# Kernel tuning notes

Hardware: AMD Instinct MI355X
Metric: run time of the kernel (lower is better)

The kernel has to match this reference:

```python
import jax, jax.numpy as jnp
import numpy as np

# SMPL kinematic tree (24 joints); parent[0] = -1 (root)
PARENT = [-1, 0, 0, 0, 1, 2, 3, 4, 5, 6, 7, 8, 9, 9, 9, 12, 13, 14, 16, 17, 18, 19, 20, 21]
J = len(PARENT)  # 24


def _ancestor_matrix(parent):
    # A[j, k] = 1 if offset k contributes to joint j (k on path root->j, excluding root)
    n = len(parent)
    A = np.zeros((n, n), dtype=np.float32)
    for j in range(1, n):
        k = j
        while k > 0:
            A[j, k] = 1.0
            k = parent[k]
    return A

ANC = jnp.asarray(_ancestor_matrix(PARENT))  # [J, J]


def setup_inputs() -> dict:
    key = jax.random.key(0)
    k0, k1, k2 = jax.random.split(key, 3)
    B, D, H = 131072, 256, 512
    out_dim = (J - 1) * 4
    z = jax.random.normal(k0, (B, D), jnp.float32)
    W1 = jax.random.normal(k1, (D, H), jnp.float32) / np.float32(np.sqrt(D))
    b1 = jnp.zeros((H,), jnp.float32)
    W2 = jax.random.normal(k2, (H, out_dim), jnp.float32) / np.float32(np.sqrt(H))
    b2 = jnp.zeros((out_dim,), jnp.float32)
    return {"z": z, "W1": W1, "b1": b1, "W2": W2, "b2": b2}


def reference(z, W1, b1, W2, b2):
    B = z.shape[0]
    h = jax.nn.silu(z @ W1 + b1)                      # [B, 512]
    raw = (h @ W2 + b2).reshape(B, J - 1, 4)          # [B, J-1, 4]
    dir_raw = raw[..., :3]                            # [B, J-1, 3]
    len_raw = raw[..., 3]                             # [B, J-1]
    # F.normalize(dim=-1, eps=1e-6): x / max(||x||, eps)
    norm = jnp.linalg.norm(dir_raw, axis=-1, keepdims=True)
    direction = dir_raw / jnp.maximum(norm, 1e-6)
    length = jax.nn.softplus(len_raw)                 # [B, J-1]
    offset_non_root = direction * length[..., None]
    offsets = jnp.concatenate(
        [jnp.zeros((B, 1, 3), z.dtype), offset_non_root], axis=1
    )  # [B, J, 3]
    # Forward kinematics: joints[j] = sum of offsets along ancestor chain.
    # The sequential per-joint loop collapses to one matmul with the
    # precomputed ancestor incidence matrix (same math, depth-parallel).
    joints = jnp.einsum('jk,bkc->bjc', ANC, offsets)  # [B, J, 3]
    return (joints, offsets, length)
```

## Files before the change

kernel.cpp:

```cpp
#include <hip/hip_runtime.h>
#include <math.h>

typedef _Float16 half8 __attribute__((ext_vector_type(8)));
typedef float floatx4 __attribute__((ext_vector_type(4)));

#define DD 256
#define HH 512
#define OC 92
#define NJ 24
#define BM 128
#define NCHUNK 16
#define W2P_OFF 131072
#define FLAG_OFF 196608
#define FCAP 16384
#define BUF_BYTES 24576

__constant__ int c_parent[NJ] = {-1,0,0,0,1,2,3,4,5,6,7,8,9,9,9,12,13,14,16,17,18,19,20,21};


__global__ __launch_bounds__(256)
void prep(const float* __restrict__ W1, const float* __restrict__ W2,
          _Float16* __restrict__ ws, int* __restrict__ flags) {
    int t = blockIdx.x * 256 + threadIdx.x;
    if (t == 0) flags[0] = 0;
    if (t < 16384) {
        int lane = t & 63;
        int cfrag = (t >> 6) & 1;
        int ks = (t >> 7) & 7;
        int ckI = t >> 10;
        int c = ckI * 32 + cfrag * 16 + (lane & 15);
        int kb = ks * 32 + 4 * (lane >> 4);
        half8 v;
        #pragma unroll
        for (int j = 0; j < 8; ++j) {
            int k = kb + (j & 3) + 16 * (j >> 2);
            v[j] = (_Float16)W1[k * HH + c];
        }
        *(half8*)(ws + t * 8) = v;
    } else {
        int u = t - 16384;
        int lane = u & 63;
        int s = (u >> 6) & 7;
        int ck = u >> 9;
        half8 v;
        if (s < 6) {
            int c = s * 16 + (lane & 15);
            int kb = ck * 32 + 4 * (lane >> 4);
            #pragma unroll
            for (int j = 0; j < 8; ++j) {
                int k = kb + (j & 3) + 16 * (j >> 2);
                v[j] = (c < OC) ? (_Float16)W2[k * OC + c] : (_Float16)0.0f;
            }
        } else {
            #pragma unroll
            for (int j = 0; j < 8; ++j) v[j] = (_Float16)0.0f;
        }
        *(half8*)(ws + W2P_OFF + ck * 4096 + (s * 64 + lane) * 8) = v;
    }
}

__global__ __launch_bounds__(256)
__attribute__((amdgpu_waves_per_eu(2, 2)))
void fused_main(const float* __restrict__ z, const _Float16* __restrict__ wsp,
                const float* __restrict__ b1, const float* __restrict__ b2,
                float* __restrict__ out, long long Btot, int* __restrict__ flags)
{
    __shared__ __align__(16) char smem[2 * BUF_BYTES + 2048 + 384];
    float* b1f = (float*)(smem + 2 * BUF_BYTES);
    float* b2f = (float*)(smem + 2 * BUF_BYTES + 2048);
    const int tid = threadIdx.x;
    const int w   = tid >> 6;
    const int l   = tid & 63;
    const int l15 = l & 15;
    const int l4  = l >> 4;

    const long long R0  = (long long)blockIdx.x * BM;
    const long long R0w = R0 + w * 32;

#define STAGE(ck_, dstbuf_) do {                                                             \
    const char* s1g_ = (const char*)wsp + (size_t)(ck_) * 16384;                             \
    const char* s2g_ = (const char*)(wsp + W2P_OFF) + (size_t)(ck_) * 8192;                  \
    _Pragma("unroll")                                                                        \
    for (int i_ = 0; i_ < 6; ++i_) {                                                         \
        int g_ = w * 6 + i_;                                                                 \
        const char* src_ = (g_ < 16) ? (s1g_ + g_ * 1024) : (s2g_ + (g_ - 16) * 1024);       \
        __builtin_amdgcn_global_load_lds(                                                    \
            (const __attribute__((address_space(1))) void*)(src_ + l * 16),                  \
            (__attribute__((address_space(3))) void*)((dstbuf_) + g_ * 1024), 16, 0, 0);     \
    }                                                                                        \
} while (0)

#define COMPUTE_CHUNK(bufc_, ck_) do {                                                       \
    const _Float16* s1_ = (const _Float16*)(bufc_);                                          \
    const _Float16* s2_ = (const _Float16*)((bufc_) + 16384);                                \
    half8 wf_[16];                                                                           \
    _Pragma("unroll")                                                                        \
    for (int f_ = 0; f_ < 16; ++f_) wf_[f_] = *(const half8*)(s1_ + (f_ * 64 + l) * 8);      \
    floatx4 vb1_[2];                                                                         \
    vb1_[0] = *(const floatx4*)(b1f + (ck_) * 32 + 4 * l4);                                  \
    vb1_[1] = *(const floatx4*)(b1f + (ck_) * 32 + 16 + 4 * l4);                             \
    floatx4 acc1_[2][2];                                                                     \
    acc1_[0][0] = (floatx4)0.0f; acc1_[0][1] = (floatx4)0.0f;                                \
    acc1_[1][0] = (floatx4)0.0f; acc1_[1][1] = (floatx4)0.0f;                                \
    _Pragma("unroll")                                                                        \
    for (int ks_ = 0; ks_ < 8; ++ks_) {                                                      \
        _Pragma("unroll")                                                                    \
        for (int cf_ = 0; cf_ < 2; ++cf_) {                                                  \
            acc1_[0][cf_] = __builtin_amdgcn_mfma_f32_16x16x32_f16(wf_[ks_ * 2 + cf_], zh[0][ks_], acc1_[0][cf_], 0, 0, 0); \
            acc1_[1][cf_] = __builtin_amdgcn_mfma_f32_16x16x32_f16(wf_[ks_ * 2 + cf_], zh[1][ks_], acc1_[1][cf_], 0, 0, 0); \
        }                                                                                    \
    }                                                                                        \
    half8 w2f_[6];                                                                           \
    _Pragma("unroll")                                                                        \
    for (int cf_ = 0; cf_ < 6; ++cf_) w2f_[cf_] = *(const half8*)(s2_ + (cf_ * 64 + l) * 8); \
    half8 ah_[2];                                                                            \
    _Pragma("unroll")                                                                        \
    for (int at_ = 0; at_ < 2; ++at_) {                                                      \
        _Pragma("unroll")                                                                    \
        for (int cf_ = 0; cf_ < 2; ++cf_) {                                                  \
            _Pragma("unroll")                                                                \
            for (int i_ = 0; i_ < 4; ++i_) {                                                 \
                float a_ = acc1_[at_][cf_][i_] + vb1_[cf_][i_];                              \
                float hv_ = a_ * __builtin_amdgcn_rcpf(1.0f + __expf(-a_));                  \
                ah_[at_][i_ | (cf_ << 2)] = (_Float16)hv_;                                   \
            }                                                                                \
        }                                                                                    \
    }                                                                                        \
    _Pragma("unroll")                                                                        \
    for (int cf_ = 0; cf_ < 6; ++cf_) {                                                      \
        a2[0][cf_] = __builtin_amdgcn_mfma_f32_16x16x32_f16(w2f_[cf_], ah_[0], a2[0][cf_], 0, 0, 0); \
        a2[1][cf_] = __builtin_amdgcn_mfma_f32_16x16x32_f16(w2f_[cf_], ah_[1], a2[1][cf_], 0, 0, 0); \
    }                                                                                        \
} while (0)

    STAGE(0, smem);
    if (tid < 128) *(floatx4*)(b1f + tid * 4) = *(const floatx4*)(b1 + tid * 4);
    if (tid >= 128 && tid < 224) { int c = tid - 128; b2f[c] = (c < OC) ? b2[c] : 0.0f; }

    half8 zh[2][8];
    #pragma unroll
    for (int at = 0; at < 2; ++at) {
        const float* zrow = z + (R0w + (long long)(at * 16 + l15)) * DD;
        #pragma unroll
        for (int ks = 0; ks < 8; ++ks) {
            const float* p = zrow + ks * 32 + l4 * 4;
            floatx4 va = *(const floatx4*)p;
            floatx4 vb = *(const floatx4*)(p + 16);
            half8 th;
            th[0] = (_Float16)va[0]; th[1] = (_Float16)va[1];
            th[2] = (_Float16)va[2]; th[3] = (_Float16)va[3];
            th[4] = (_Float16)vb[0]; th[5] = (_Float16)vb[1];
            th[6] = (_Float16)vb[2]; th[7] = (_Float16)vb[3];
            zh[at][ks] = th;
        }
    }

    floatx4 a2[2][6];
    #pragma unroll
    for (int at = 0; at < 2; ++at)
        #pragma unroll
        for (int i = 0; i < 6; ++i) a2[at][i] = (floatx4)0.0f;

    __syncthreads();

    #pragma unroll 1
    for (int t = 0; t < 8; ++t) {
        STAGE(2 * t + 1, smem + BUF_BYTES);
        COMPUTE_CHUNK(smem, 2 * t);
        asm volatile("s_waitcnt vmcnt(0)" ::: "memory");
        __builtin_amdgcn_s_barrier();
        if (t < 7) STAGE(2 * t + 2, smem);
        COMPUTE_CHUNK(smem + BUF_BYTES, 2 * t + 1);
        asm volatile("s_waitcnt vmcnt(0)" ::: "memory");
        __builtin_amdgcn_s_barrier();
    }

    float* s_off = (float*)smem + w * 3040;
    float* s_len = s_off + 2304;

    #pragma unroll
    for (int at = 0; at < 2; ++at) {
        const int r = at * 16 + l15;
        #pragma unroll
        for (int cf = 0; cf < 6; ++cf) {
            const int j = 4 * cf + l4;
            if (j < NJ - 1) {
                float x  = a2[at][cf][0] + b2f[4 * j + 0];
                float y  = a2[at][cf][1] + b2f[4 * j + 1];
                float zz = a2[at][cf][2] + b2f[4 * j + 2];
                float lr = a2[at][cf][3] + b2f[4 * j + 3];
                float nrm = sqrtf(x * x + y * y + zz * zz);
                float inv = __builtin_amdgcn_rcpf(fmaxf(nrm, 1e-6f));
                float len = fmaxf(lr, 0.0f) + __logf(1.0f + __expf(-fabsf(lr)));
                if (len > 12.0f * nrm) {
                    int fi = atomicAdd(&flags[0], 1);
                    if (fi < FCAP) flags[1 + fi] = (int)(R0w + r);
                }
                s_off[r * 72 + 3 * (j + 1) + 0] = x * inv * len;
                s_off[r * 72 + 3 * (j + 1) + 1] = y * inv * len;
                s_off[r * 72 + 3 * (j + 1) + 2] = zz * inv * len;
                s_len[r * 23 + j] = len;
            }
        }
    }
    if (l < 32) {
        s_off[l * 72 + 0] = 0.0f;
        s_off[l * 72 + 1] = 0.0f;
        s_off[l * 72 + 2] = 0.0f;
    }
    __syncthreads();

    float* joints  = out;
    float* offsets = out + Btot * (NJ * 3);
    float* length  = out + 2 * Btot * (NJ * 3);

    {
        float* gdst = offsets + R0w * (NJ * 3);
        #pragma unroll
        for (int t4 = 0; t4 < 9; ++t4) {
            int idx = (t4 * 64 + l) * 4;
            *(float4*)(gdst + idx) = *(float4*)(s_off + idx);
        }
    }
    {
        float* gdst = length + R0w * (NJ - 1);
        for (int t4 = l; t4 < 184; t4 += 64) {
            *(float4*)(gdst + t4 * 4) = *(float4*)(s_len + t4 * 4);
        }
    }
    for (int task = l; task < 32 * NJ; task += 64) {
        int r = task / NJ;
        int j = task - r * NJ;
        float jx = 0.0f, jy = 0.0f, jz = 0.0f;
        int k = j;
        while (k > 0) {
            jx += s_off[r * 72 + 3 * k + 0];
            jy += s_off[r * 72 + 3 * k + 1];
            jz += s_off[r * 72 + 3 * k + 2];
            k = c_parent[k];
        }
        long long base = (R0w + r) * (NJ * 3) + j * 3;
        joints[base + 0] = jx;
        joints[base + 1] = jy;
        joints[base + 2] = jz;
    }
#undef STAGE
#undef COMPUTE_CHUNK
}

__global__ __launch_bounds__(256)
void fixup(const float* __restrict__ z, const float* __restrict__ W1,
           const float* __restrict__ b1, const float* __restrict__ W2,
           const float* __restrict__ b2, float* __restrict__ out,
           long long Btot, const int* __restrict__ flags)
{
    __shared__ float z_s[DD];
    __shared__ float h_s[HH];
    __shared__ float raw_s[96];
    __shared__ float off_s[72];
    int n = flags[0];
    if (n > FCAP) n = FCAP;
    if ((int)blockIdx.x >= n) return;
    const int tid = threadIdx.x;
    const long long row = flags[1 + blockIdx.x];

    float* joints  = out;
    float* offsets = out + Btot * (NJ * 3);
    float* length  = out + 2 * Btot * (NJ * 3);

    z_s[tid] = z[row * DD + tid];
    __syncthreads();
    for (int c = tid; c < HH; c += 256) {
        float acc = b1[c];
        for (int k = 0; k < DD; ++k) acc = fmaf(z_s[k], W1[k * HH + c], acc);
        h_s[c] = acc / (1.0f + expf(-acc));
    }
    __syncthreads();
    if (tid < OC) {
        float acc = b2[tid];
        for (int k = 0; k < HH; ++k) acc = fmaf(h_s[k], W2[k * OC + tid], acc);
        raw_s[tid] = acc;
    }
    __syncthreads();
    if (tid < NJ - 1) {
        int j = tid;
        float x  = raw_s[4 * j + 0];
        float y  = raw_s[4 * j + 1];
        float zz = raw_s[4 * j + 2];
        float lr = raw_s[4 * j + 3];
        float nrm = sqrtf(x * x + y * y + zz * zz);
        float inv = 1.0f / fmaxf(nrm, 1e-6f);
        float len = fmaxf(lr, 0.0f) + log1pf(expf(-fabsf(lr)));
        off_s[3 * (j + 1) + 0] = x * inv * len;
        off_s[3 * (j + 1) + 1] = y * inv * len;
        off_s[3 * (j + 1) + 2] = zz * inv * len;
        length[row * (NJ - 1) + j] = len;
    }
    if (tid < 3) off_s[tid] = 0.0f;
    __syncthreads();
    if (tid < NJ) {
        int j = tid;
        float jx = 0.0f, jy = 0.0f, jz = 0.0f;
        int k = j;
        while (k > 0) {
            jx += off_s[3 * k + 0];
            jy += off_s[3 * k + 1];
            jz += off_s[3 * k + 2];
            k = c_parent[k];
        }
        joints[row * (NJ * 3) + j * 3 + 0] = jx;
        joints[row * (NJ * 3) + j * 3 + 1] = jy;
        joints[row * (NJ * 3) + j * 3 + 2] = jz;
    }
    if (tid < NJ * 3) offsets[row * (NJ * 3) + tid] = off_s[tid];
}

extern "C" void kernel_launch(void* const* d_in, const int* in_sizes, int n_in,
                              void* d_out, int out_size, void* d_ws, size_t ws_size,
                              hipStream_t stream) {
    const float* z  = (const float*)d_in[0];
    const float* W1 = (const float*)d_in[1];
    const float* b1 = (const float*)d_in[2];
    const float* W2 = (const float*)d_in[3];
    const float* b2 = (const float*)d_in[4];
    float* out = (float*)d_out;
    _Float16* ws = (_Float16*)d_ws;
    int* flags = (int*)(ws + FLAG_OFF);

    const long long Btot = (long long)in_sizes[0] / DD;

    prep<<<96, 256, 0, stream>>>(W1, W2, ws, flags);
    fused_main<<<(int)(Btot / BM), 256, 0, stream>>>(z, ws, b1, b2, out, Btot, flags);
    fixup<<<4096, 256, 0, stream>>>(z, W1, b1, W2, b2, out, Btot, flags);
}
```

Before: 148.6 us.

## Read W2 fragments from global memory and shrink LDS to raise occupancy

W2 fragments are no longer staged through LDS. Each chunk loads them straight from global/L2, and the packed W2 layout drops its padding slots. This shrinks the per-buffer LDS footprint so more blocks can be resident, and the waves-per-EU hint is relaxed from exactly 2 to at least 4. The epilogue now reuses the smaller LDS in two halves, serialized by a barrier, which adds epilogue latency and puts global loads inside the compute loop.

```diff
diff --git a/kernel.cpp b/kernel.cpp
--- a/kernel.cpp
+++ b/kernel.cpp
@@ -10,10 +10,10 @@
 #define NJ 24
 #define BM 128
 #define NCHUNK 16
-#define W2P_OFF 131072
-#define FLAG_OFF 196608
+#define W2_OFF 131072
+#define FLAG_OFF 180224
 #define FCAP 16384
-#define BUF_BYTES 24576
+#define BUF_BYTES 16384
 
 __constant__ int c_parent[NJ] = {-1,0,0,0,1,2,3,4,5,6,7,8,9,9,9,12,13,14,16,17,18,19,20,21};
 
@@ -37,30 +37,26 @@
             v[j] = (_Float16)W1[k * HH + c];
         }
         *(half8*)(ws + t * 8) = v;
-    } else {
+    } else if (t < 16384 + 6144) {
         int u = t - 16384;
         int lane = u & 63;
-        int s = (u >> 6) & 7;
-        int ck = u >> 9;
+        int rest = u >> 6;
+        int cfrag = rest % 6;
+        int ckI = rest / 6;
+        int c = cfrag * 16 + (lane & 15);
+        int kb = ckI * 32 + 4 * (lane >> 4);
         half8 v;
-        if (s < 6) {
-            int c = s * 16 + (lane & 15);
-            int kb = ck * 32 + 4 * (lane >> 4);
-            #pragma unroll
-            for (int j = 0; j < 8; ++j) {
-                int k = kb + (j & 3) + 16 * (j >> 2);
-                v[j] = (c < OC) ? (_Float16)W2[k * OC + c] : (_Float16)0.0f;
-            }
-        } else {
-            #pragma unroll
-            for (int j = 0; j < 8; ++j) v[j] = (_Float16)0.0f;
+        #pragma unroll
+        for (int j = 0; j < 8; ++j) {
+            int k = kb + (j & 3) + 16 * (j >> 2);
+            v[j] = (c < OC) ? (_Float16)W2[k * OC + c] : (_Float16)0.0f;
         }
-        *(half8*)(ws + W2P_OFF + ck * 4096 + (s * 64 + lane) * 8) = v;
+        *(half8*)(ws + W2_OFF + (ckI * 6 + cfrag) * 512 + lane * 8) = v;
     }
 }
 
 __global__ __launch_bounds__(256)
-__attribute__((amdgpu_waves_per_eu(2, 2)))
+__attribute__((amdgpu_waves_per_eu(4)))
 void fused_main(const float* __restrict__ z, const _Float16* __restrict__ wsp,
                 const float* __restrict__ b1, const float* __restrict__ b2,
                 float* __restrict__ out, long long Btot, int* __restrict__ flags)
@@ -79,26 +75,22 @@
 
 #define STAGE(ck_, dstbuf_) do {                                                             \
     const char* s1g_ = (const char*)wsp + (size_t)(ck_) * 16384;                             \
-    const char* s2g_ = (const char*)(wsp + W2P_OFF) + (size_t)(ck_) * 8192;                  \
-    _Pragma("unroll")                                                                        \
-    for (int i_ = 0; i_ < 6; ++i_) {                                                         \
-        int g_ = w * 6 + i_;                                                                 \
-        const char* src_ = (g_ < 16) ? (s1g_ + g_ * 1024) : (s2g_ + (g_ - 16) * 1024);       \
+    _Pragma("unroll")                                                                        \
+    for (int i_ = 0; i_ < 4; ++i_) {                                                         \
+        int g_ = w * 4 + i_;                                                                 \
         __builtin_amdgcn_global_load_lds(                                                    \
-            (const __attribute__((address_space(1))) void*)(src_ + l * 16),                  \
+            (const __attribute__((address_space(1))) void*)(s1g_ + g_ * 1024 + l * 16),      \
             (__attribute__((address_space(3))) void*)((dstbuf_) + g_ * 1024), 16, 0, 0);     \
     }                                                                                        \
 } while (0)
+
+#define MF(a_, b_, c_) __builtin_amdgcn_mfma_f32_16x16x32_f16((a_), (b_), (c_), 0, 0, 0)
 
 #define COMPUTE_CHUNK(bufc_, ck_) do {                                                       \
     const _Float16* s1_ = (const _Float16*)(bufc_);                                          \
-    const _Float16* s2_ = (const _Float16*)((bufc_) + 16384);                                \
     half8 wf_[16];                                                                           \
     _Pragma("unroll")                                                                        \
     for (int f_ = 0; f_ < 16; ++f_) wf_[f_] = *(const half8*)(s1_ + (f_ * 64 + l) * 8);      \
-    floatx4 vb1_[2];                                                                         \
-    vb1_[0] = *(const floatx4*)(b1f + (ck_) * 32 + 4 * l4);                                  \
-    vb1_[1] = *(const floatx4*)(b1f + (ck_) * 32 + 16 + 4 * l4);                             \
     floatx4 acc1_[2][2];                                                                     \
     acc1_[0][0] = (floatx4)0.0f; acc1_[0][1] = (floatx4)0.0f;                                \
     acc1_[1][0] = (floatx4)0.0f; acc1_[1][1] = (floatx4)0.0f;                                \
@@ -106,13 +98,16 @@
     for (int ks_ = 0; ks_ < 8; ++ks_) {                                                      \
         _Pragma("unroll")                                                                    \
         for (int cf_ = 0; cf_ < 2; ++cf_) {                                                  \
-            acc1_[0][cf_] = __builtin_amdgcn_mfma_f32_16x16x32_f16(wf_[ks_ * 2 + cf_], zh[0][ks_], acc1_[0][cf_], 0, 0, 0); \
-            acc1_[1][cf_] = __builtin_amdgcn_mfma_f32_16x16x32_f16(wf_[ks_ * 2 + cf_], zh[1][ks_], acc1_[1][cf_], 0, 0, 0); \
-        }                                                                                    \
-    }                                                                                        \
+            acc1_[0][cf_] = MF(wf_[ks_ * 2 + cf_], zh[0][ks_], acc1_[0][cf_]);               \
+            acc1_[1][cf_] = MF(wf_[ks_ * 2 + cf_], zh[1][ks_], acc1_[1][cf_]);               \
+        }                                                                                    \
+    }                                                                                        \
+    const _Float16* p2_ = wsp + W2_OFF + (ck_) * 3072 + l * 8;                               \
     half8 w2f_[6];                                                                           \
     _Pragma("unroll")                                                                        \
-    for (int cf_ = 0; cf_ < 6; ++cf_) w2f_[cf_] = *(const half8*)(s2_ + (cf_ * 64 + l) * 8); \
+    for (int cf_ = 0; cf_ < 6; ++cf_) w2f_[cf_] = *(const half8*)(p2_ + cf_ * 512);          \
+    floatx4 vb1a_ = *(const floatx4*)(b1f + (ck_) * 32 + 4 * l4);                            \
+    floatx4 vb1b_ = *(const floatx4*)(b1f + (ck_) * 32 + 16 + 4 * l4);                       \
     half8 ah_[2];                                                                            \
     _Pragma("unroll")                                                                        \
     for (int at_ = 0; at_ < 2; ++at_) {                                                      \
@@ -120,7 +115,7 @@
         for (int cf_ = 0; cf_ < 2; ++cf_) {                                                  \
             _Pragma("unroll")                                                                \
             for (int i_ = 0; i_ < 4; ++i_) {                                                 \
-                float a_ = acc1_[at_][cf_][i_] + vb1_[cf_][i_];                              \
+                float a_ = acc1_[at_][cf_][i_] + (cf_ ? vb1b_[i_] : vb1a_[i_]);              \
                 float hv_ = a_ * __builtin_amdgcn_rcpf(1.0f + __expf(-a_));                  \
                 ah_[at_][i_ | (cf_ << 2)] = (_Float16)hv_;                                   \
             }                                                                                \
@@ -128,8 +123,72 @@
     }                                                                                        \
     _Pragma("unroll")                                                                        \
     for (int cf_ = 0; cf_ < 6; ++cf_) {                                                      \
-        a2[0][cf_] = __builtin_amdgcn_mfma_f32_16x16x32_f16(w2f_[cf_], ah_[0], a2[0][cf_], 0, 0, 0); \
-        a2[1][cf_] = __builtin_amdgcn_mfma_f32_16x16x32_f16(w2f_[cf_], ah_[1], a2[1][cf_], 0, 0, 0); \
+        a2[0][cf_] = MF(w2f_[cf_], ah_[0], a2[0][cf_]);                                      \
+        a2[1][cf_] = MF(w2f_[cf_], ah_[1], a2[1][cf_]);                                      \
+    }                                                                                        \
+} while (0)
+
+#define EPILOGUE(region_) do {                                                               \
+    float* s_off_ = (float*)(smem + (region_) * 12160);                                      \
+    float* s_len_ = s_off_ + 2304;                                                           \
+    _Pragma("unroll")                                                                        \
+    for (int at_ = 0; at_ < 2; ++at_) {                                                      \
+        const int r_ = at_ * 16 + l15;                                                       \
+        _Pragma("unroll")                                                                    \
+        for (int cf_ = 0; cf_ < 6; ++cf_) {                                                  \
+            const int j_ = 4 * cf_ + l4;                                                     \
+            if (j_ < NJ - 1) {                                                               \
+                float x_  = a2[at_][cf_][0] + b2f[4 * j_ + 0];                               \
+                float y_  = a2[at_][cf_][1] + b2f[4 * j_ + 1];                               \
+                float zz_ = a2[at_][cf_][2] + b2f[4 * j_ + 2];                               \
+                float lr_ = a2[at_][cf_][3] + b2f[4 * j_ + 3];                               \
+                float nrm_ = sqrtf(x_ * x_ + y_ * y_ + zz_ * zz_);                           \
+                float inv_ = __builtin_amdgcn_rcpf(fmaxf(nrm_, 1e-6f));                      \
+                float len_ = fmaxf(lr_, 0.0f) + __logf(1.0f + __expf(-fabsf(lr_)));          \
+                if (len_ > 12.0f * nrm_) {                                                   \
+                    int fi_ = atomicAdd(&flags[0], 1);                                       \
+                    if (fi_ < FCAP) flags[1 + fi_] = (int)(R0w + r_);                        \
+                }                                                                            \
+                s_off_[r_ * 72 + 3 * (j_ + 1) + 0] = x_ * inv_ * len_;                       \
+                s_off_[r_ * 72 + 3 * (j_ + 1) + 1] = y_ * inv_ * len_;                       \
+                s_off_[r_ * 72 + 3 * (j_ + 1) + 2] = zz_ * inv_ * len_;                      \
+                s_len_[r_ * 23 + j_] = len_;                                                 \
+            }                                                                                \
+        }                                                                                    \
+    }                                                                                        \
+    if (l < 32) {                                                                            \
+        s_off_[l * 72 + 0] = 0.0f;                                                           \
+        s_off_[l * 72 + 1] = 0.0f;                                                           \
+        s_off_[l * 72 + 2] = 0.0f;                                                           \
+    }                                                                                        \
+    {                                                                                        \
+        float* gdst_ = offsets + R0w * (NJ * 3);                                             \
+        _Pragma("unroll")                                                                    \
+        for (int t4_ = 0; t4_ < 9; ++t4_) {                                                  \
+            int idx_ = (t4_ * 64 + l) * 4;                                                   \
+            *(float4*)(gdst_ + idx_) = *(float4*)(s_off_ + idx_);                            \
+        }                                                                                    \
+    }                                                                                        \
+    {                                                                                        \
+        float* gdst_ = length + R0w * (NJ - 1);                                              \
+        for (int t4_ = l; t4_ < 184; t4_ += 64)                                              \
+            *(float4*)(gdst_ + t4_ * 4) = *(float4*)(s_len_ + t4_ * 4);                      \
+    }                                                                                        \
+    for (int task_ = l; task_ < 32 * NJ; task_ += 64) {                                      \
+        int r_ = task_ / NJ;                                                                 \
+        int j_ = task_ - r_ * NJ;                                                            \
+        float jx_ = 0.0f, jy_ = 0.0f, jz_ = 0.0f;                                            \
+        int k_ = j_;                                                                         \
+        while (k_ > 0) {                                                                     \
+            jx_ += s_off_[r_ * 72 + 3 * k_ + 0];                                             \
+            jy_ += s_off_[r_ * 72 + 3 * k_ + 1];                                             \
+            jz_ += s_off_[r_ * 72 + 3 * k_ + 2];                                             \
+            k_ = c_parent[k_];                                                               \
+        }                                                                                    \
+        long long base_ = (R0w + r_) * (NJ * 3) + j_ * 3;                                    \
+        joints[base_ + 0] = jx_;                                                             \
+        joints[base_ + 1] = jy_;                                                             \
+        joints[base_ + 2] = jz_;                                                             \
     }                                                                                        \
 } while (0)
 
@@ -175,77 +234,18 @@
         __builtin_amdgcn_s_barrier();
     }
 
-    float* s_off = (float*)smem + w * 3040;
-    float* s_len = s_off + 2304;
-
-    #pragma unroll
-    for (int at = 0; at < 2; ++at) {
-        const int r = at * 16 + l15;
-        #pragma unroll
-        for (int cf = 0; cf < 6; ++cf) {
-            const int j = 4 * cf + l4;
-            if (j < NJ - 1) {
-                float x  = a2[at][cf][0] + b2f[4 * j + 0];
-                float y  = a2[at][cf][1] + b2f[4 * j + 1];
-                float zz = a2[at][cf][2] + b2f[4 * j + 2];
-                float lr = a2[at][cf][3] + b2f[4 * j + 3];
-                float nrm = sqrtf(x * x + y * y + zz * zz);
-                float inv = __builtin_amdgcn_rcpf(fmaxf(nrm, 1e-6f));
-                float len = fmaxf(lr, 0.0f) + __logf(1.0f + __expf(-fabsf(lr)));
-                if (len > 12.0f * nrm) {
-                    int fi = atomicAdd(&flags[0], 1);
-                    if (fi < FCAP) flags[1 + fi] = (int)(R0w + r);
-                }
-                s_off[r * 72 + 3 * (j + 1) + 0] = x * inv * len;
-                s_off[r * 72 + 3 * (j + 1) + 1] = y * inv * len;
-                s_off[r * 72 + 3 * (j + 1) + 2] = zz * inv * len;
-                s_len[r * 23 + j] = len;
-            }
-        }
-    }
-    if (l < 32) {
-        s_off[l * 72 + 0] = 0.0f;
-        s_off[l * 72 + 1] = 0.0f;
-        s_off[l * 72 + 2] = 0.0f;
-    }
-    __syncthreads();
-
     float* joints  = out;
     float* offsets = out + Btot * (NJ * 3);
     float* length  = out + 2 * Btot * (NJ * 3);
 
-    {
-        float* gdst = offsets + R0w * (NJ * 3);
-        #pragma unroll
-        for (int t4 = 0; t4 < 9; ++t4) {
-            int idx = (t4 * 64 + l) * 4;
-            *(float4*)(gdst + idx) = *(float4*)(s_off + idx);
-        }
-    }
-    {
-        float* gdst = length + R0w * (NJ - 1);
-        for (int t4 = l; t4 < 184; t4 += 64) {
-            *(float4*)(gdst + t4 * 4) = *(float4*)(s_len + t4 * 4);
-        }
-    }
-    for (int task = l; task < 32 * NJ; task += 64) {
-        int r = task / NJ;
-        int j = task - r * NJ;
-        float jx = 0.0f, jy = 0.0f, jz = 0.0f;
-        int k = j;
-        while (k > 0) {
-            jx += s_off[r * 72 + 3 * k + 0];
-            jy += s_off[r * 72 + 3 * k + 1];
-            jz += s_off[r * 72 + 3 * k + 2];
-            k = c_parent[k];
-        }
-        long long base = (R0w + r) * (NJ * 3) + j * 3;
-        joints[base + 0] = jx;
-        joints[base + 1] = jy;
-        joints[base + 2] = jz;
-    }
+    if (w < 2) EPILOGUE(w);
+    __syncthreads();
+    if (w >= 2) EPILOGUE(w - 2);
+
 #undef STAGE
 #undef COMPUTE_CHUNK
+#undef EPILOGUE
+#undef MF
 }
 
 __global__ __launch_bounds__(256)
@@ -329,7 +329,7 @@
 
     const long long Btot = (long long)in_sizes[0] / DD;
 
-    prep<<<96, 256, 0, stream>>>(W1, W2, ws, flags);
+    prep<<<88, 256, 0, stream>>>(W1, W2, ws, flags);
     fused_main<<<(int)(Btot / BM), 256, 0, stream>>>(z, ws, b1, b2, out, Btot, flags);
     fixup<<<4096, 256, 0, stream>>>(z, W1, b1, W2, b2, out, Btot, flags);
 }
```

New measurement: 359.0 us. +141.6%, slower.
